# Optimization experiments

Measured on AMD Instinct MI355X. Metric: run time of the kernel, lower is better.

The kernel has to match this reference:

```python
import jax, jax.numpy as jnp
import numpy as np

STRIDES = (8.0, 16.0, 32.0)
NC, DFL = 80, 16
NO = NC + 4 * DFL            # 144
TOPK, ALPHA, BETA, EPS = 10, 0.5, 6.0, 1e-9
MAXB = 32                    # static max gt boxes per image (pad rows are masked out)
W_CLS, W_BOX, W_DFL = 0.5, 7.5, 1.5
B, IMG, NT = 16, 640, 256


def _make_anchors(shapes, strides, offset=0.5):
    pts, strs = [], []
    for (h, w), s in zip(shapes, strides):
        sx = jnp.arange(w, dtype=jnp.float32) + offset
        sy = jnp.arange(h, dtype=jnp.float32) + offset
        gy, gx = jnp.meshgrid(sy, sx, indexing='ij')
        pts.append(jnp.stack([gx, gy], -1).reshape(-1, 2))
        strs.append(jnp.full((h * w, 1), s, dtype=jnp.float32))
    return jnp.concatenate(pts, 0), jnp.concatenate(strs, 0)


def _ciou(box1, box2, eps=1e-7):
    b1x1, b1y1, b1x2, b1y2 = jnp.split(box1, 4, -1)
    b2x1, b2y1, b2x2, b2y2 = jnp.split(box2, 4, -1)
    w1, h1 = b1x2 - b1x1, b1y2 - b1y1 + eps
    w2, h2 = b2x2 - b2x1, b2y2 - b2y1 + eps
    inter = (jnp.maximum(jnp.minimum(b1x2, b2x2) - jnp.maximum(b1x1, b2x1), 0.0) *
             jnp.maximum(jnp.minimum(b1y2, b2y2) - jnp.maximum(b1y1, b2y1), 0.0))
    union = w1 * h1 + w2 * h2 - inter + eps
    iou = inter / union
    cw = jnp.maximum(b1x2, b2x2) - jnp.minimum(b1x1, b2x1)
    ch = jnp.maximum(b1y2, b2y2) - jnp.minimum(b1y1, b2y1)
    c2 = cw ** 2 + ch ** 2 + eps
    rho2 = ((b2x1 + b2x2 - b1x1 - b1x2) ** 2 + (b2y1 + b2y2 - b1y1 - b1y2) ** 2) / 4
    v = (4.0 / np.pi ** 2) * (jnp.arctan(w2 / h2) - jnp.arctan(w1 / h1)) ** 2
    a = jax.lax.stop_gradient(v / (v - iou + (1.0 + eps)))
    return iou - (rho2 / c2 + v * a)     # [..., 1]


def _assign(scores, bboxes, gt_labels, gt_bboxes, mask_gt, anchors):
    # Task-aligned assigner (YOLOv8 TAL). All inputs are gradient-stopped.
    b, a, c = scores.shape
    n = gt_bboxes.shape[1]
    lt, rb = gt_bboxes[..., :2], gt_bboxes[..., 2:]
    deltas = jnp.concatenate([anchors[None, None] - lt[:, :, None],
                              rb[:, :, None] - anchors[None, None]], -1)        # [b,n,a,4]
    mask_in_gts = (deltas.min(-1) > EPS).astype(scores.dtype)                   # [b,n,a]
    overlaps = jnp.maximum(_ciou(gt_bboxes[:, :, None], bboxes[:, None])[..., 0], 0.0)
    labels = gt_labels[..., 0].astype(jnp.int32)                                # [b,n]
    bbox_scores = jax.vmap(lambda s, l: jnp.take(s, l, axis=1).T)(scores, labels)  # [b,n,a]
    align = bbox_scores ** ALPHA * overlaps ** BETA
    mask_true = mask_in_gts * mask_gt                                           # [b,n,a]
    metrics = align * mask_true
    tkv, tki = jax.lax.top_k(metrics, TOPK)                                     # [b,n,k]
    valid = jnp.max(tkv, -1, keepdims=True) > EPS
    tki = jnp.where(valid, tki, 0)
    bi = jnp.arange(b)[:, None, None]
    ni = jnp.arange(n)[None, :, None]
    cnt = jnp.zeros((b, n, a), scores.dtype).at[bi, ni, tki].add(1.0)
    mask_topk = jnp.where(cnt > 1, 0.0, cnt)
    mask_pos = mask_topk * mask_true
    fg = mask_pos.sum(1)                                                        # [b,a]
    multi = (fg > 1)[:, None, :]
    is_max = jnp.transpose(jax.nn.one_hot(jnp.argmax(overlaps, 1), n, dtype=scores.dtype), (0, 2, 1))
    mask_pos = jnp.where(multi, is_max, mask_pos)
    fg = mask_pos.sum(1)
    tgi = jnp.argmax(mask_pos, 1)                                               # [b,a]
    t_labels = jnp.take_along_axis(labels, tgi, axis=1)
    t_bboxes = jnp.take_along_axis(gt_bboxes, jnp.broadcast_to(tgi[..., None], (b, a, 4)), axis=1)
    t_scores = jax.nn.one_hot(jnp.maximum(t_labels, 0), NC, dtype=scores.dtype) * (fg > 0)[..., None]
    align = align * mask_pos
    pos_align = jnp.max(align, -1, keepdims=True)                               # [b,n,1]
    pos_ovl = jnp.max(overlaps * mask_pos, -1, keepdims=True)
    norm = jnp.max(align * pos_ovl / (pos_align + EPS), 1)[..., None]           # [b,a,1]
    return t_bboxes, t_scores * norm, fg > 0


def _forward(p3, p4, p5, targets):
    x = [jnp.transpose(o, (0, 3, 1, 2)) for o in (p3, p4, p5)]                  # NCHW
    b = x[0].shape[0]
    out = jnp.concatenate([o.reshape(b, NO, -1) for o in x], 2)
    pred_dist = jnp.transpose(out[:, :4 * DFL], (0, 2, 1))                      # [b,A,64]
    pred_scores = jnp.transpose(out[:, 4 * DFL:], (0, 2, 1))                    # [b,A,80]
    shapes = [o.shape[2:4] for o in x]
    size = jnp.array(shapes[0], jnp.float32) * STRIDES[0]                       # [H, W] pixels
    anchor_points, stride_tensor = _make_anchors(shapes, STRIDES)
    # per-image padded gt tensor (vectorized replacement of the TF scatter loop)
    img = targets[:, 0].astype(jnp.int32)
    nt = targets.shape[0]
    pos = jnp.arange(nt)
    rank = jnp.sum((img[None, :] == img[:, None]) & (pos[None, :] < pos[:, None]), 1)
    gt = jnp.zeros((b, MAXB, 5), jnp.float32).at[img, rank].set(targets[:, 1:])
    scale = jnp.stack([size[1], size[0], size[1], size[0]])
    xywh = gt[..., 1:5] * scale
    gt_bboxes = jnp.concatenate([xywh[..., :2] - xywh[..., 2:] / 2,
                                 xywh[..., :2] + xywh[..., 2:] / 2], -1)
    gt_labels = gt[..., 0:1]
    mask_gt = (jnp.sum(gt_bboxes, 2, keepdims=True) > 0).astype(jnp.float32)    # [b,n,1]
    a_num = pred_dist.shape[1]
    project = jnp.arange(DFL, dtype=jnp.float32)
    pd = jax.nn.softmax(pred_dist.reshape(b, a_num, 4, DFL), -1)
    pd = jnp.einsum('bafc,c->baf', pd, project)                                 # DFL expectation
    pred_bboxes = jnp.concatenate([anchor_points - pd[..., :2],
                                   anchor_points + pd[..., 2:]], -1)            # [b,A,4]
    scores = jax.lax.stop_gradient(jax.nn.sigmoid(pred_scores))
    bboxes = jax.lax.stop_gradient(pred_bboxes * stride_tensor)
    t_bboxes, t_scores, fg = _assign(scores, bboxes, gt_labels, gt_bboxes, mask_gt,
                                     anchor_points * stride_tensor)
    t_bboxes = t_bboxes / stride_tensor
    tss = jnp.maximum(jnp.sum(t_scores), 1.0)
    z, l = t_scores, pred_scores
    bce = jnp.maximum(l, 0.0) - l * z + jnp.log1p(jnp.exp(-jnp.abs(l)))
    loss_cls = jnp.sum(bce) / tss
    fgf = fg.astype(jnp.float32)
    weight = jnp.sum(t_scores, -1) * fgf                                        # [b,A], 0 off-fg
    iou = _ciou(pred_bboxes, t_bboxes)[..., 0]
    loss_box = jnp.sum((1.0 - iou) * weight) / tss
    lt_rb = jnp.concatenate([anchor_points - t_bboxes[..., :2],
                             t_bboxes[..., 2:] - anchor_points], -1)
    lt_rb = jnp.clip(lt_rb, 0.0, DFL - 1.01)                                    # [b,A,4]
    logp = jax.nn.log_softmax(pred_dist.reshape(b, a_num, 4, DFL), -1)
    tl = lt_rb.astype(jnp.int32)
    wl = (tl + 1).astype(jnp.float32) - lt_rb
    left = -jnp.take_along_axis(logp, tl[..., None], -1)[..., 0]
    right = -jnp.take_along_axis(logp, (tl + 1)[..., None], -1)[..., 0]
    dfl = jnp.mean(left * wl + right * (1.0 - wl), -1)                          # [b,A]
    loss_dfl = jnp.sum(dfl * weight) / tss
    return W_CLS * loss_cls + W_BOX * loss_box + W_DFL * loss_dfl


def setup_inputs() -> dict:
    key = jax.random.key(0)
    k1, k2, k3, k4, k5, k6 = jax.random.split(key, 6)
    p3 = jax.random.normal(k1, (B, IMG // 8, IMG // 8, NO), jnp.float32)
    p4 = jax.random.normal(k2, (B, IMG // 16, IMG // 16, NO), jnp.float32)
    p5 = jax.random.normal(k3, (B, IMG // 32, IMG // 32, NO), jnp.float32)
    img = (jnp.arange(NT) % B).astype(jnp.float32)        # exactly 16 boxes / image <= MAXB
    cls = jax.random.randint(k4, (NT,), 0, NC).astype(jnp.float32)
    xy = jax.random.uniform(k5, (NT, 2), minval=0.25, maxval=0.75)
    wh = jax.random.uniform(k6, (NT, 2), minval=0.05, maxval=0.30)
    targets = jnp.concatenate([img[:, None], cls[:, None], xy, wh], -1)   # [NT,6]
    return {"p3": p3, "p4": p4, "p5": p5, "targets": targets}


def reference(p3, p4, p5, targets):
    return _forward(p3, p4, p5, targets)
```

## Files before the change

### kernel.cpp

```cpp
#include <hip/hip_runtime.h>
#include <math.h>

#define A_TOT 8400
#define NB 16
#define NG 32
#define NCH 144
#define NDFL 16
#define EPSF 1e-9f
#define CEPS 1e-7f
#define INV_PI2_4 0.40528473456935109f
#define NBLK2 2100
#define LSEG 512
#define K56_BLOCKS 32
#define K4CAP 1024

#define LOADU(p)  __hip_atomic_load((p), __ATOMIC_ACQUIRE, __HIP_MEMORY_SCOPE_AGENT)
#define LOADF(p)  __hip_atomic_load((p), __ATOMIC_ACQUIRE, __HIP_MEMORY_SCOPE_AGENT)

#define OFF_GTBOX   0
#define OFF_GTLAB   2048
#define OFF_MASKGT  2560
#define OFF_ATANGT  3072
#define OFF_ACC     3584
#define OFF_CTRL    3592
#define OFF_BCNT    3600
#define OFF_PART2   3856
#define OFF_PART6   5968
#define OFF_POSM    6224
#define OFF_PBOX    10320
#define OFF_MPOS    547920
#define OFF_LIST    682320

__device__ __forceinline__ void locate(int a, int& loc, int& W, float& s, int& lvl, int& hw){
  if (a < 6400)      { lvl = 0; loc = a;        W = 80; s = 8.f;  hw = 6400; }
  else if (a < 8000) { lvl = 1; loc = a - 6400; W = 40; s = 16.f; hw = 1600; }
  else               { lvl = 2; loc = a - 8000; W = 20; s = 32.f; hw = 400;  }
}

__device__ __forceinline__ const float* level_ptr(const float* p3, const float* p4, const float* p5, int lvl){
  return lvl == 0 ? p3 : (lvl == 1 ? p4 : p5);
}

__device__ __forceinline__ float ciou_gp(float gx1,float gy1,float gx2,float gy2,float atg,
                                         float px1,float py1,float px2,float py2,float atp){
  float w1 = gx2-gx1, h1 = gy2-gy1+CEPS;
  float w2 = px2-px1, h2 = py2-py1+CEPS;
  float iw = fmaxf(fminf(gx2,px2)-fmaxf(gx1,px1), 0.f);
  float ih = fmaxf(fminf(gy2,py2)-fmaxf(gy1,py1), 0.f);
  float inter = iw*ih;
  float uni = w1*h1 + w2*h2 - inter + CEPS;
  float iou = inter/uni;
  float cw = fmaxf(gx2,px2)-fminf(gx1,px1);
  float ch = fmaxf(gy2,py2)-fminf(gy1,py1);
  float c2 = cw*cw + ch*ch + CEPS;
  float dx = px1+px2-gx1-gx2, dy = py1+py2-gy1-gy2;
  float rho2 = (dx*dx + dy*dy)*0.25f;
  float dv = atp - atg;
  float v = INV_PI2_4*dv*dv;
  float al = v/(v - iou + (1.f + CEPS));
  return iou - (rho2/c2 + v*al);
}

__global__ __launch_bounds__(256) void k2x(const float* __restrict__ p3, const float* __restrict__ p4,
                          const float* __restrict__ p5, const float* __restrict__ tgt, int nt,
                          float* __restrict__ ws){
  int tid = threadIdx.x;
  int bx = blockIdx.x;
  if (bx == NBLK2){
    __shared__ int simg[256];
    float* gtbox  = ws + OFF_GTBOX;
    int*   gtlab  = (int*)(ws + OFF_GTLAB);
    float* maskgt = ws + OFF_MASKGT;
    float* atangt = ws + OFF_ATANGT;
    for (int i = tid; i < NB*NG*4; i += 256) gtbox[i] = 0.f;
    for (int i = tid; i < NB*NG; i += 256) gtlab[i] = 0;
    if (tid < 8){ (ws + OFF_ACC)[tid] = 0.f; ((unsigned*)(ws + OFF_CTRL))[tid] = 0u; }
    for (int i = tid; i < 256;  i += 256) ((unsigned*)(ws + OFF_BCNT))[i] = 0u;
    for (int i = tid; i < NB*NG*8; i += 256) (ws + OFF_POSM)[i] = 0.f;
    for (int i = tid; i < nt && i < 256; i += 256) simg[i] = (int)tgt[i*6];
    __syncthreads();
    for (int i = tid; i < nt && i < 256; i += 256){
      int b = simg[i];
      int r = 0;
      for (int j = 0; j < i; j++) r += (simg[j] == b);
      if (b >= 0 && b < NB && r < NG){
        float cls = tgt[i*6+1];
        float cx = tgt[i*6+2]*640.f, cy = tgt[i*6+3]*640.f;
        float w  = tgt[i*6+4]*640.f, h  = tgt[i*6+5]*640.f;
        int o = (b*NG + r)*4;
        gtbox[o+0] = cx - 0.5f*w; gtbox[o+1] = cy - 0.5f*h;
        gtbox[o+2] = cx + 0.5f*w; gtbox[o+3] = cy + 0.5f*h;
        gtlab[b*NG + r] = (int)cls;
      }
    }
    __syncthreads();
    for (int i = tid; i < NB*NG; i += 256){
      float x1 = gtbox[i*4], y1 = gtbox[i*4+1], x2 = gtbox[i*4+2], y2 = gtbox[i*4+3];
      maskgt[i] = ((x1+y1+x2+y2) > 0.f) ? 1.f : 0.f;
      atangt[i] = atanf((x2-x1)/(y2-y1+CEPS));
    }
    return;
  }
  __shared__ float redw[4];
  {
    int mp = bx*256 + tid;
    if (mp < NB*A_TOT) ((unsigned*)(ws + OFF_MPOS))[mp] = 0u;
  }
  const float* base; int grow0, hw, W, lvloff;
  if (bx < 1600)      { base = p3; grow0 = bx*64;        hw = 6400; W = 80; lvloff = 0; }
  else if (bx < 2000) { base = p4; grow0 = (bx-1600)*64; hw = 1600; W = 40; lvloff = 6400; }
  else                { base = p5; grow0 = (bx-2000)*64; hw = 400;  W = 20; lvloff = 8000; }

  const float4* src = (const float4*)base + (size_t)grow0*36;
  {
    int r = tid >> 2, f = tid & 3;
    const float4* rp = src + r*36 + f*4;
    float4 v0 = rp[0], v1 = rp[1], v2 = rp[2], v3 = rp[3];
    float m = v0.x;
    m = fmaxf(m, v0.y); m = fmaxf(m, v0.z); m = fmaxf(m, v0.w);
    m = fmaxf(m, v1.x); m = fmaxf(m, v1.y); m = fmaxf(m, v1.z); m = fmaxf(m, v1.w);
    m = fmaxf(m, v2.x); m = fmaxf(m, v2.y); m = fmaxf(m, v2.z); m = fmaxf(m, v2.w);
    m = fmaxf(m, v3.x); m = fmaxf(m, v3.y); m = fmaxf(m, v3.z); m = fmaxf(m, v3.w);
    float e, se, swe;
    e = __expf(v0.x - m); se = e;            swe = 0.f;
    e = __expf(v0.y - m); se += e;           swe += e;
    e = __expf(v0.z - m); se += e;           swe = fmaf(2.f,  e, swe);
    e = __expf(v0.w - m); se += e;           swe = fmaf(3.f,  e, swe);
    e = __expf(v1.x - m); se += e;           swe = fmaf(4.f,  e, swe);
    e = __expf(v1.y - m); se += e;           swe = fmaf(5.f,  e, swe);
    e = __expf(v1.z - m); se += e;           swe = fmaf(6.f,  e, swe);
    e = __expf(v1.w - m); se += e;           swe = fmaf(7.f,  e, swe);
    e = __expf(v2.x - m); se += e;           swe = fmaf(8.f,  e, swe);
    e = __expf(v2.y - m); se += e;           swe = fmaf(9.f,  e, swe);
    e = __expf(v2.z - m); se += e;           swe = fmaf(10.f, e, swe);
    e = __expf(v2.w - m); se += e;           swe = fmaf(11.f, e, swe);
    e = __expf(v3.x - m); se += e;           swe = fmaf(12.f, e, swe);
    e = __expf(v3.y - m); se += e;           swe = fmaf(13.f, e, swe);
    e = __expf(v3.z - m); se += e;           swe = fmaf(14.f, e, swe);
    e = __expf(v3.w - m); se += e;           swe = fmaf(15.f, e, swe);
    float pdf = __fdividef(swe, se);
    float s1 = __shfl_xor(pdf, 1);
    float s2 = __shfl_xor(pdf, 2);
    float s3 = __shfl_xor(pdf, 3);
    if (f == 0){
      int grow = grow0 + r;
      int b = grow / hw, loc = grow - b*hw;
      float ax = (loc % W) + 0.5f, ay = (loc / W) + 0.5f;
      float4 pb;
      pb.x = ax - pdf; pb.y = ay - s1; pb.z = ax + s2; pb.w = ay + s3;
      ((float4*)(ws + OFF_PBOX))[(size_t)b*A_TOT + lvloff + loc] = pb;
    }
  }
  float sp = 0.f;
  #pragma unroll
  for (int i = 0; i < 5; i++){
    int id = i*256 + tid;
    int r = id/20, q = id - r*20;
    float4 v = src[r*36 + 16 + q];
    #pragma unroll
    for (int e2 = 0; e2 < 4; e2++){
      float x = (&v.x)[e2];
      float ex = __expf(-fabsf(x));
      sp += fmaxf(x, 0.f) + __logf(1.f + ex);
    }
  }
  #pragma unroll
  for (int st = 1; st < 64; st <<= 1) sp += __shfl_xor(sp, st);
  int wid = tid >> 6, lane = tid & 63;
  if (lane == 0) redw[wid] = sp;
  __syncthreads();
  if (tid == 0) (ws + OFF_PART2)[bx] = redw[0]+redw[1]+redw[2]+redw[3];
}

__global__ __launch_bounds__(256) void k4x(const float* __restrict__ p3, const float* __restrict__ p4,
                        const float* __restrict__ p5, float* __restrict__ ws){
  __shared__ unsigned long long wtop[4*10];
  int tid = threadIdx.x;
  int lane = tid & 63, wid = tid >> 6;
  int bx = blockIdx.x;
  int b = bx >> 5, n = bx & 31;
  float mk = ws[OFF_MASKGT + b*NG + n];
  if (mk <= 0.f) return;
  int lab = ((const int*)(ws + OFF_GTLAB))[b*NG + n];
  int ch = 64 + lab;
  float atg = ws[OFF_ATANGT + b*NG + n];
  const float* gt = ws + OFF_GTBOX + (b*NG + n)*4;
  float gx1 = gt[0], gy1 = gt[1], gx2 = gt[2], gy2 = gt[3];

  int clo0 = max(0, (int)floorf(gx1*0.125f   - 0.5f));
  int chi0 = min(79,(int)ceilf (gx2*0.125f   - 0.5f));
  int rlo0 = max(0, (int)floorf(gy1*0.125f   - 0.5f));
  int rhi0 = min(79,(int)ceilf (gy2*0.125f   - 0.5f));
  int clo1 = max(0, (int)floorf(gx1*0.0625f  - 0.5f));
  int chi1 = min(39,(int)ceilf (gx2*0.0625f  - 0.5f));
  int rlo1 = max(0, (int)floorf(gy1*0.0625f  - 0.5f));
  int rhi1 = min(39,(int)ceilf (gy2*0.0625f  - 0.5f));
  int clo2 = max(0, (int)floorf(gx1*0.03125f - 0.5f));
  int chi2 = min(19,(int)ceilf (gx2*0.03125f - 0.5f));
  int rlo2 = max(0, (int)floorf(gy1*0.03125f - 0.5f));
  int rhi2 = min(19,(int)ceilf (gy2*0.03125f - 0.5f));
  int nc0 = chi0-clo0+1, nr0 = rhi0-rlo0+1;
  int nc1 = chi1-clo1+1, nr1 = rhi1-rlo1+1;
  int nc2 = chi2-clo2+1, nr2 = rhi2-rlo2+1;
  int cnt0 = (nc0>0 && nr0>0) ? nc0*nr0 : 0;
  int cnt1 = (nc1>0 && nr1>0) ? nc1*nr1 : 0;
  int cnt2 = (nc2>0 && nr2>0) ? nc2*nr2 : 0;
  if (16+cnt0 > K4CAP)           cnt0 = K4CAP-16;
  if (16+cnt0+cnt1 > K4CAP)      cnt1 = K4CAP-16-cnt0;
  if (16+cnt0+cnt1+cnt2 > K4CAP) cnt2 = K4CAP-16-cnt0-cnt1;
  int b1 = 16 + cnt0, b2 = b1 + cnt1;
  int tot = b2 + cnt2;

  unsigned long long key[4];
  #pragma unroll
  for (int j = 0; j < 4; j++){
    key[j] = 0ull;
    int c = j*256 + tid;
    if (c < tot){
      int aidx, loc, W, hw; float s; const float* bp; bool dup = false;
      if (c < 16)     { aidx = c; loc = c; W = 80; s = 8.f;  hw = 6400; bp = p3; }
      else if (c < b1){ int jj = c-16; int rr = jj/nc0; loc = (rlo0+rr)*80 + clo0 + (jj - rr*nc0);
                        aidx = loc;        W = 80; s = 8.f;  hw = 6400; bp = p3; dup = (aidx < 16); }
      else if (c < b2){ int jj = c-b1; int rr = jj/nc1; loc = (rlo1+rr)*40 + clo1 + (jj - rr*nc1);
                        aidx = 6400 + loc; W = 40; s = 16.f; hw = 1600; bp = p4; }
      else            { int jj = c-b2; int rr = jj/nc2; loc = (rlo2+rr)*20 + clo2 + (jj - rr*nc2);
                        aidx = 8000 + loc; W = 20; s = 32.f; hw = 400;  bp = p5; }
      if (!dup){
        float m = 0.f;
        float axi = ((loc % W) + 0.5f)*s, ayi = ((loc / W) + 0.5f)*s;
        float dmin = fminf(fminf(axi-gx1, ayi-gy1), fminf(gx2-axi, gy2-ayi));
        if (dmin > EPSF){
          float4 pg = ((const float4*)(ws + OFF_PBOX))[(size_t)b*A_TOT + aidx];
          float px1 = pg.x*s, py1 = pg.y*s, px2 = pg.z*s, py2 = pg.w*s;
          float atp = atanf((px2-px1)/(py2-py1+CEPS));
          float o = fmaxf(ciou_gp(gx1,gy1,gx2,gy2,atg, px1,py1,px2,py2,atp), 0.f);
          float l = bp[((size_t)b*hw + loc)*NCH + ch];
          float sc = __frcp_rn(1.f + __expf(-l));
          float o2 = o*o;
          m = sqrtf(sc)*o2*o2*o2;
        }
        key[j] = ((unsigned long long)__float_as_uint(m) << 32)
               | (unsigned long long)(0xFFFFFFFFu - (unsigned)aidx);
      }
    }
  }
  for (int k = 0; k < 10; k++){
    unsigned long long bk = key[0];
    #pragma unroll
    for (int j = 1; j < 4; j++) if (key[j] > bk) bk = key[j];
    #pragma unroll
    for (int st = 1; st < 64; st <<= 1){
      unsigned long long ok = __shfl_xor(bk, st);
      if (ok > bk) bk = ok;
    }
    if (lane == 0) wtop[wid*10 + k] = bk;
    #pragma unroll
    for (int j = 0; j < 4; j++) if (key[j] == bk) key[j] = 0ull;
  }
  __syncthreads();
  if (wid == 0){
    unsigned long long mk64 = (lane < 40) ? wtop[lane] : 0ull;
    float top0m = 0.f;
    int mytop = -1;
    for (int k = 0; k < 10; k++){
      unsigned long long bk = mk64;
      #pragma unroll
      for (int st = 1; st < 64; st <<= 1){
        unsigned long long ok = __shfl_xor(bk, st);
        if (ok > bk) bk = ok;
      }
      if (k == 0) top0m = __uint_as_float((unsigned)(bk >> 32));
      if (lane == k) mytop = (int)(0xFFFFFFFFu - (unsigned)(bk & 0xFFFFFFFFull));
      if (mk64 == bk) mk64 = 0ull;
    }
    bool want = (lane < 10) && (top0m > EPSF) && (mytop >= 0) && (mytop < A_TOT);
    if (want){
      int loc, W, lvl, hw; float s;
      locate(mytop, loc, W, s, lvl, hw);
      float axi = ((loc % W) + 0.5f)*s, ayi = ((loc / W) + 0.5f)*s;
      float dmin = fminf(fminf(axi-gx1, ayi-gy1), fminf(gx2-axi, gy2-ayi));
      want = (dmin > EPSF);
    }
    unsigned old = 0u;
    if (want) old = atomicOr((unsigned*)(ws + OFF_MPOS) + (size_t)b*A_TOT + mytop, 1u << n);
    bool w2 = want && (old == 0u);
    unsigned long long m64 = __ballot(w2);
    if (w2){
      int lead = __ffsll((long long)m64) - 1;
      unsigned base = 0;
      if (lane == lead) base = atomicAdd((unsigned*)(ws + OFF_BCNT) + b*16, (unsigned)__popcll(m64));
      base = __shfl(base, lead);
      unsigned slot = base + (unsigned)__popcll(m64 & ((1ull << lane) - 1ull));
      if (slot < LSEG) ((unsigned*)(ws + OFF_LIST))[b*LSEG + slot] = (unsigned)mytop;
    }
  }
}

__global__ __launch_bounds__(256) void k56x(const float* __restrict__ p3, const float* __restrict__ p4,
                        const float* __restrict__ p5, float* __restrict__ ws, float* __restrict__ out){
  __shared__ float redw[16];
  __shared__ float fin[4];
  __shared__ int lastf;
  __shared__ unsigned cnt_s;
  int tid = threadIdx.x;
  int lane = tid & 63, wid = tid >> 6;
  int s_id = blockIdx.x*256 + tid;
  int b = s_id >> 9, i = s_id & (LSEG-1);
  if (tid == 0) cnt_s = (b < NB) ? LOADU((unsigned*)(ws + OFF_BCNT) + b*16) : 0u;
  __syncthreads();
  unsigned cntb = cnt_s;
  bool valid = false; int a = 0;
  if (b < NB && (unsigned)i < cntb && cntb <= LSEG){
    valid = true;
    a = (int)((unsigned*)(ws + OFF_LIST))[b*LSEG + i];
  }
  int ns = 0; float av = 0.f;
  int loc=0, W=80, lvl=0, hw=6400; float sfac=8.f;
  if (valid){
    unsigned bits = ((const unsigned*)(ws + OFF_MPOS))[(size_t)b*A_TOT + a];
    locate(a, loc, W, sfac, lvl, hw);
    float4 pg = ((const float4*)(ws + OFF_PBOX))[(size_t)b*A_TOT + a];
    float px1 = pg.x*sfac, py1 = pg.y*sfac, px2 = pg.z*sfac, py2 = pg.w*sfac;
    float atp = atanf((px2-px1)/(py2-py1+CEPS));
    if (__popc(bits) == 1){ ns = __ffs(bits) - 1; }
    else {
      float bv = -1.f; ns = 0;
      for (int nn = 0; nn < NG; nn++){
        const float* g = ws + OFF_GTBOX + (b*NG + nn)*4;
        float atg = ws[OFF_ATANGT + b*NG + nn];
        float o = fmaxf(ciou_gp(g[0],g[1],g[2],g[3],atg, px1,py1,px2,py2,atp), 0.f);
        if (o > bv){ bv = o; ns = nn; }
      }
    }
    const float* g = ws + OFF_GTBOX + (b*NG + ns)*4;
    float atg = ws[OFF_ATANGT + b*NG + ns];
    float o = fmaxf(ciou_gp(g[0],g[1],g[2],g[3],atg, px1,py1,px2,py2,atp), 0.f);
    int lab = ((const int*)(ws + OFF_GTLAB))[b*NG + ns];
    float l = level_ptr(p3,p4,p5,lvl)[((size_t)b*hw + loc)*NCH + 64 + lab];
    float sc = __frcp_rn(1.f + __expf(-l));
    float o2 = o*o;
    av = sqrtf(sc)*o2*o2*o2;
    unsigned* pm = (unsigned*)(ws + OFF_POSM) + (b*NG + ns)*8;
    atomicMax(pm + 0, __float_as_uint(av));
    atomicMax(pm + 1, __float_as_uint(o));
  }
  if (blockIdx.x == 0){
    float v = 0.f;
    for (int j = tid; j < NBLK2; j += 256) v += (ws + OFF_PART2)[j];
    #pragma unroll
    for (int st = 1; st < 64; st <<= 1) v += __shfl_xor(v, st);
    if (lane == 0) redw[wid] = v;
    __syncthreads();
    if (tid == 0)
      __hip_atomic_store(ws + OFF_ACC + 0, redw[0]+redw[1]+redw[2]+redw[3],
                         __ATOMIC_RELEASE, __HIP_MEMORY_SCOPE_AGENT);
    __syncthreads();
  }
  __syncthreads();
  if (tid == 0){
    __threadfence();
    __hip_atomic_fetch_add((unsigned*)(ws + OFF_CTRL) + 1, 1u,
                           __ATOMIC_ACQ_REL, __HIP_MEMORY_SCOPE_AGENT);
    while (LOADU((unsigned*)(ws + OFF_CTRL) + 1) < K56_BLOCKS){ __builtin_amdgcn_s_sleep(1); }
  }
  __syncthreads();
  __threadfence();
  float bcec = 0.f, boxl = 0.f, dfll = 0.f, tsc = 0.f;
  if (valid){
    unsigned* pm = (unsigned*)(ws + OFF_POSM) + (b*NG + ns)*8;
    float pa = __uint_as_float(LOADU(pm + 0));
    float po = __uint_as_float(LOADU(pm + 1));
    float norm = av * po / (pa + EPSF);
    const float* row = level_ptr(p3,p4,p5,lvl) + ((size_t)b*hw + loc)*NCH;
    int lab = ((const int*)(ws + OFF_GTLAB))[b*NG + ns];
    if (lab < 0) lab = 0;
    tsc = norm;
    bcec = -row[64 + lab]*norm;
    float4 pb = ((const float4*)(ws + OFF_PBOX))[(size_t)b*A_TOT + a];
    const float* g = ws + OFF_GTBOX + (b*NG + ns)*4;
    float inv_s = 1.f/sfac;
    float tx1 = g[0]*inv_s, ty1 = g[1]*inv_s, tx2 = g[2]*inv_s, ty2 = g[3]*inv_s;
    float w1 = pb.z-pb.x, h1 = pb.w-pb.y+CEPS;
    float w2 = tx2-tx1,   h2 = ty2-ty1+CEPS;
    float iw = fmaxf(fminf(pb.z,tx2)-fmaxf(pb.x,tx1), 0.f);
    float ih = fmaxf(fminf(pb.w,ty2)-fmaxf(pb.y,ty1), 0.f);
    float inter = iw*ih;
    float uni = w1*h1 + w2*h2 - inter + CEPS;
    float iou = inter/uni;
    float cw = fmaxf(pb.z,tx2)-fminf(pb.x,tx1);
    float ch = fmaxf(pb.w,ty2)-fminf(pb.y,ty1);
    float c2 = cw*cw + ch*ch + CEPS;
    float dx = tx1+tx2-pb.x-pb.z, dy = ty1+ty2-pb.y-pb.w;
    float rho2 = (dx*dx + dy*dy)*0.25f;
    float dv = atanf(w2/h2) - atanf(w1/h1);
    float v = INV_PI2_4*dv*dv;
    float al = v/(v - iou + (1.f + CEPS));
    float ci = iou - (rho2/c2 + v*al);
    boxl = (1.f - ci)*norm;
    float ax = (loc % W) + 0.5f, ay = (loc / W) + 0.5f;
    float ltrb[4] = {ax - tx1, ay - ty1, tx2 - ax, ty2 - ay};
    float ds = 0.f;
    #pragma unroll
    for (int f = 0; f < 4; f++){
      float val = fminf(fmaxf(ltrb[f], 0.f), (float)NDFL - 1.01f);
      int tl = (int)val;
      float wl = (float)(tl + 1) - val;
      float x[16];
      const float4* r4 = (const float4*)(row + f*16);
      #pragma unroll
      for (int q = 0; q < 4; q++){ float4 vv = r4[q]; x[q*4]=vv.x; x[q*4+1]=vv.y; x[q*4+2]=vv.z; x[q*4+3]=vv.w; }
      float m = x[0];
      #pragma unroll
      for (int j = 1; j < 16; j++) m = fmaxf(m, x[j]);
      float se = 0.f;
      #pragma unroll
      for (int j = 0; j < 16; j++) se += __expf(x[j]-m);
      float lse = m + __logf(se);
      float xl = 0.f, xr = 0.f;
      #pragma unroll
      for (int j = 0; j < 16; j++){
        xl = (j == tl)   ? x[j] : xl;
        xr = (j == tl+1) ? x[j] : xr;
      }
      ds += (lse - xl)*wl + (lse - xr)*(1.f - wl);
    }
    dfll = ds*0.25f*norm;
  }
  float vals[4] = {bcec, boxl, dfll, tsc};
  #pragma unroll
  for (int q = 0; q < 4; q++){
    float v = vals[q];
    #pragma unroll
    for (int st = 1; st < 64; st <<= 1) v += __shfl_xor(v, st);
    if (lane == 0) redw[wid*4 + q] = v;
  }
  if (tid == 0) lastf = 0;
  __syncthreads();
  if (tid < 4){
    float v = redw[tid] + redw[4+tid] + redw[8+tid] + redw[12+tid];
    __hip_atomic_store(ws + OFF_PART6 + blockIdx.x*4 + tid, v,
                       __ATOMIC_RELEASE, __HIP_MEMORY_SCOPE_AGENT);
  }
  __syncthreads();
  if (tid == 0){
    __threadfence();
    unsigned tkt = __hip_atomic_fetch_add((unsigned*)(ws + OFF_CTRL) + 2, 1u,
                                          __ATOMIC_ACQ_REL, __HIP_MEMORY_SCOPE_AGENT);
    if (tkt == K56_BLOCKS - 1) lastf = 1;
  }
  __syncthreads();
  if (lastf){
    if (tid < 4) fin[tid] = 0.f;
    __syncthreads();
    if (tid < 4*K56_BLOCKS){
      float v = LOADF(ws + OFF_PART6 + tid);
      atomicAdd(&fin[tid & 3], v);
    }
    __syncthreads();
    if (tid == 0){
      float sp = LOADF(ws + OFF_ACC + 0);
      float tss = fmaxf(fin[3], 1.f);
      out[0] = (0.5f*(sp + fin[0]) + 7.5f*fin[1] + 1.5f*fin[2]) / tss;
    }
  }
}

extern "C" void kernel_launch(void* const* d_in, const int* in_sizes, int n_in,
                              void* d_out, int out_size, void* d_ws, size_t ws_size,
                              hipStream_t stream) {
  const float* p3 = (const float*)d_in[0];
  const float* p4 = (const float*)d_in[1];
  const float* p5 = (const float*)d_in[2];
  const float* tg = (const float*)d_in[3];
  int nt = in_sizes[3] / 6;
  float* ws = (float*)d_ws;
  float* out = (float*)d_out;

  k2x<<<NBLK2 + 1, 256, 0, stream>>>(p3, p4, p5, tg, nt, ws);
  k4x<<<NB*NG, 256, 0, stream>>>(p3, p4, p5, ws);
  k56x<<<K56_BLOCKS, 256, 0, stream>>>(p3, p4, p5, ws, out);
}
```

Before: 62.84 us.

## Fuse top-k assignment and loss kernels with a grid-wide arrival barrier

Merges the per-GT top-k selection kernel (512 blocks) and the loss kernel (32 blocks) into one launch. The first 32 blocks wait on a set of 16 padded arrival counters until all 512 blocks finish the top-k phase, then run the loss stage. This removes a kernel launch and its inter-kernel gap. The cost is spin-waiting blocks, and correctness depends on all 512 blocks being co-resident or scheduled before the waiters starve them.

New measurement: 85.98 us. +36.8%, slower.

```diff
diff --git a/kernel.cpp b/kernel.cpp
--- a/kernel.cpp
+++ b/kernel.cpp
@@ -11,6 +11,7 @@
 #define INV_PI2_4 0.40528473456935109f
 #define NBLK2 2100
 #define LSEG 512
+#define K46_BLOCKS 512
 #define K56_BLOCKS 32
 #define K4CAP 1024
 
@@ -24,12 +25,13 @@
 #define OFF_ACC     3584
 #define OFF_CTRL    3592
 #define OFF_BCNT    3600
-#define OFF_PART2   3856
-#define OFF_PART6   5968
-#define OFF_POSM    6224
-#define OFF_PBOX    10320
-#define OFF_MPOS    547920
-#define OFF_LIST    682320
+#define OFF_ARR     3856
+#define OFF_PART2   4112
+#define OFF_PART6   6224
+#define OFF_POSM    6352
+#define OFF_PBOX    10448
+#define OFF_MPOS    548048
+#define OFF_LIST    682448
 
 __device__ __forceinline__ void locate(int a, int& loc, int& W, float& s, int& lvl, int& hw){
   if (a < 6400)      { lvl = 0; loc = a;        W = 80; s = 8.f;  hw = 6400; }
@@ -75,7 +77,7 @@
     for (int i = tid; i < NB*NG*4; i += 256) gtbox[i] = 0.f;
     for (int i = tid; i < NB*NG; i += 256) gtlab[i] = 0;
     if (tid < 8){ (ws + OFF_ACC)[tid] = 0.f; ((unsigned*)(ws + OFF_CTRL))[tid] = 0u; }
-    for (int i = tid; i < 256;  i += 256) ((unsigned*)(ws + OFF_BCNT))[i] = 0u;
+    for (int i = tid; i < 512;  i += 256) ((unsigned*)(ws + OFF_BCNT))[i] = 0u;
     for (int i = tid; i < NB*NG*8; i += 256) (ws + OFF_POSM)[i] = 0.f;
     for (int i = tid; i < nt && i < 256; i += 256) simg[i] = (int)tgt[i*6];
     __syncthreads();
@@ -172,139 +174,153 @@
   if (tid == 0) (ws + OFF_PART2)[bx] = redw[0]+redw[1]+redw[2]+redw[3];
 }
 
-__global__ __launch_bounds__(256) void k4x(const float* __restrict__ p3, const float* __restrict__ p4,
-                        const float* __restrict__ p5, float* __restrict__ ws){
+__global__ __launch_bounds__(256) void k46(const float* __restrict__ p3, const float* __restrict__ p4,
+                        const float* __restrict__ p5, float* __restrict__ ws, float* __restrict__ out){
   __shared__ unsigned long long wtop[4*10];
-  int tid = threadIdx.x;
-  int lane = tid & 63, wid = tid >> 6;
-  int bx = blockIdx.x;
-  int b = bx >> 5, n = bx & 31;
-  float mk = ws[OFF_MASKGT + b*NG + n];
-  if (mk <= 0.f) return;
-  int lab = ((const int*)(ws + OFF_GTLAB))[b*NG + n];
-  int ch = 64 + lab;
-  float atg = ws[OFF_ATANGT + b*NG + n];
-  const float* gt = ws + OFF_GTBOX + (b*NG + n)*4;
-  float gx1 = gt[0], gy1 = gt[1], gx2 = gt[2], gy2 = gt[3];
-
-  int clo0 = max(0, (int)floorf(gx1*0.125f   - 0.5f));
-  int chi0 = min(79,(int)ceilf (gx2*0.125f   - 0.5f));
-  int rlo0 = max(0, (int)floorf(gy1*0.125f   - 0.5f));
-  int rhi0 = min(79,(int)ceilf (gy2*0.125f   - 0.5f));
-  int clo1 = max(0, (int)floorf(gx1*0.0625f  - 0.5f));
-  int chi1 = min(39,(int)ceilf (gx2*0.0625f  - 0.5f));
-  int rlo1 = max(0, (int)floorf(gy1*0.0625f  - 0.5f));
-  int rhi1 = min(39,(int)ceilf (gy2*0.0625f  - 0.5f));
-  int clo2 = max(0, (int)floorf(gx1*0.03125f - 0.5f));
-  int chi2 = min(19,(int)ceilf (gx2*0.03125f - 0.5f));
-  int rlo2 = max(0, (int)floorf(gy1*0.03125f - 0.5f));
-  int rhi2 = min(19,(int)ceilf (gy2*0.03125f - 0.5f));
-  int nc0 = chi0-clo0+1, nr0 = rhi0-rlo0+1;
-  int nc1 = chi1-clo1+1, nr1 = rhi1-rlo1+1;
-  int nc2 = chi2-clo2+1, nr2 = rhi2-rlo2+1;
-  int cnt0 = (nc0>0 && nr0>0) ? nc0*nr0 : 0;
-  int cnt1 = (nc1>0 && nr1>0) ? nc1*nr1 : 0;
-  int cnt2 = (nc2>0 && nr2>0) ? nc2*nr2 : 0;
-  if (16+cnt0 > K4CAP)           cnt0 = K4CAP-16;
-  if (16+cnt0+cnt1 > K4CAP)      cnt1 = K4CAP-16-cnt0;
-  if (16+cnt0+cnt1+cnt2 > K4CAP) cnt2 = K4CAP-16-cnt0-cnt1;
-  int b1 = 16 + cnt0, b2 = b1 + cnt1;
-  int tot = b2 + cnt2;
-
-  unsigned long long key[4];
-  #pragma unroll
-  for (int j = 0; j < 4; j++){
-    key[j] = 0ull;
-    int c = j*256 + tid;
-    if (c < tot){
-      int aidx, loc, W, hw; float s; const float* bp; bool dup = false;
-      if (c < 16)     { aidx = c; loc = c; W = 80; s = 8.f;  hw = 6400; bp = p3; }
-      else if (c < b1){ int jj = c-16; int rr = jj/nc0; loc = (rlo0+rr)*80 + clo0 + (jj - rr*nc0);
-                        aidx = loc;        W = 80; s = 8.f;  hw = 6400; bp = p3; dup = (aidx < 16); }
-      else if (c < b2){ int jj = c-b1; int rr = jj/nc1; loc = (rlo1+rr)*40 + clo1 + (jj - rr*nc1);
-                        aidx = 6400 + loc; W = 40; s = 16.f; hw = 1600; bp = p4; }
-      else            { int jj = c-b2; int rr = jj/nc2; loc = (rlo2+rr)*20 + clo2 + (jj - rr*nc2);
-                        aidx = 8000 + loc; W = 20; s = 32.f; hw = 400;  bp = p5; }
-      if (!dup){
-        float m = 0.f;
-        float axi = ((loc % W) + 0.5f)*s, ayi = ((loc / W) + 0.5f)*s;
-        float dmin = fminf(fminf(axi-gx1, ayi-gy1), fminf(gx2-axi, gy2-ayi));
-        if (dmin > EPSF){
-          float4 pg = ((const float4*)(ws + OFF_PBOX))[(size_t)b*A_TOT + aidx];
-          float px1 = pg.x*s, py1 = pg.y*s, px2 = pg.z*s, py2 = pg.w*s;
-          float atp = atanf((px2-px1)/(py2-py1+CEPS));
-          float o = fmaxf(ciou_gp(gx1,gy1,gx2,gy2,atg, px1,py1,px2,py2,atp), 0.f);
-          float l = bp[((size_t)b*hw + loc)*NCH + ch];
-          float sc = __frcp_rn(1.f + __expf(-l));
-          float o2 = o*o;
-          m = sqrtf(sc)*o2*o2*o2;
-        }
-        key[j] = ((unsigned long long)__float_as_uint(m) << 32)
-               | (unsigned long long)(0xFFFFFFFFu - (unsigned)aidx);
-      }
-    }
-  }
-  for (int k = 0; k < 10; k++){
-    unsigned long long bk = key[0];
-    #pragma unroll
-    for (int j = 1; j < 4; j++) if (key[j] > bk) bk = key[j];
-    #pragma unroll
-    for (int st = 1; st < 64; st <<= 1){
-      unsigned long long ok = __shfl_xor(bk, st);
-      if (ok > bk) bk = ok;
-    }
-    if (lane == 0) wtop[wid*10 + k] = bk;
-    #pragma unroll
-    for (int j = 0; j < 4; j++) if (key[j] == bk) key[j] = 0ull;
-  }
-  __syncthreads();
-  if (wid == 0){
-    unsigned long long mk64 = (lane < 40) ? wtop[lane] : 0ull;
-    float top0m = 0.f;
-    int mytop = -1;
-    for (int k = 0; k < 10; k++){
-      unsigned long long bk = mk64;
-      #pragma unroll
-      for (int st = 1; st < 64; st <<= 1){
-        unsigned long long ok = __shfl_xor(bk, st);
-        if (ok > bk) bk = ok;
-      }
-      if (k == 0) top0m = __uint_as_float((unsigned)(bk >> 32));
-      if (lane == k) mytop = (int)(0xFFFFFFFFu - (unsigned)(bk & 0xFFFFFFFFull));
-      if (mk64 == bk) mk64 = 0ull;
-    }
-    bool want = (lane < 10) && (top0m > EPSF) && (mytop >= 0) && (mytop < A_TOT);
-    if (want){
-      int loc, W, lvl, hw; float s;
-      locate(mytop, loc, W, s, lvl, hw);
-      float axi = ((loc % W) + 0.5f)*s, ayi = ((loc / W) + 0.5f)*s;
-      float dmin = fminf(fminf(axi-gx1, ayi-gy1), fminf(gx2-axi, gy2-ayi));
-      want = (dmin > EPSF);
-    }
-    unsigned old = 0u;
-    if (want) old = atomicOr((unsigned*)(ws + OFF_MPOS) + (size_t)b*A_TOT + mytop, 1u << n);
-    bool w2 = want && (old == 0u);
-    unsigned long long m64 = __ballot(w2);
-    if (w2){
-      int lead = __ffsll((long long)m64) - 1;
-      unsigned base = 0;
-      if (lane == lead) base = atomicAdd((unsigned*)(ws + OFF_BCNT) + b*16, (unsigned)__popcll(m64));
-      base = __shfl(base, lead);
-      unsigned slot = base + (unsigned)__popcll(m64 & ((1ull << lane) - 1ull));
-      if (slot < LSEG) ((unsigned*)(ws + OFF_LIST))[b*LSEG + slot] = (unsigned)mytop;
-    }
-  }
-}
-
-__global__ __launch_bounds__(256) void k56x(const float* __restrict__ p3, const float* __restrict__ p4,
-                        const float* __restrict__ p5, float* __restrict__ ws, float* __restrict__ out){
   __shared__ float redw[16];
   __shared__ float fin[4];
   __shared__ int lastf;
   __shared__ unsigned cnt_s;
   int tid = threadIdx.x;
   int lane = tid & 63, wid = tid >> 6;
-  int s_id = blockIdx.x*256 + tid;
+  int bx = blockIdx.x;
+
+  {
+    int b = bx >> 5, n = bx & 31;
+    float mk = ws[OFF_MASKGT + b*NG + n];
+    if (mk > 0.f){
+      int lab = ((const int*)(ws + OFF_GTLAB))[b*NG + n];
+      int ch = 64 + lab;
+      float atg = ws[OFF_ATANGT + b*NG + n];
+      const float* gt = ws + OFF_GTBOX + (b*NG + n)*4;
+      float gx1 = gt[0], gy1 = gt[1], gx2 = gt[2], gy2 = gt[3];
+      int clo0 = max(0, (int)floorf(gx1*0.125f   - 0.5f));
+      int chi0 = min(79,(int)ceilf (gx2*0.125f   - 0.5f));
+      int rlo0 = max(0, (int)floorf(gy1*0.125f   - 0.5f));
+      int rhi0 = min(79,(int)ceilf (gy2*0.125f   - 0.5f));
+      int clo1 = max(0, (int)floorf(gx1*0.0625f  - 0.5f));
+      int chi1 = min(39,(int)ceilf (gx2*0.0625f  - 0.5f));
+      int rlo1 = max(0, (int)floorf(gy1*0.0625f  - 0.5f));
+      int rhi1 = min(39,(int)ceilf (gy2*0.0625f  - 0.5f));
+      int clo2 = max(0, (int)floorf(gx1*0.03125f - 0.5f));
+      int chi2 = min(19,(int)ceilf (gx2*0.03125f - 0.5f));
+      int rlo2 = max(0, (int)floorf(gy1*0.03125f - 0.5f));
+      int rhi2 = min(19,(int)ceilf (gy2*0.03125f - 0.5f));
+      int nc0 = chi0-clo0+1, nr0 = rhi0-rlo0+1;
+      int nc1 = chi1-clo1+1, nr1 = rhi1-rlo1+1;
+      int nc2 = chi2-clo2+1, nr2 = rhi2-rlo2+1;
+      int cnt0 = (nc0>0 && nr0>0) ? nc0*nr0 : 0;
+      int cnt1 = (nc1>0 && nr1>0) ? nc1*nr1 : 0;
+      int cnt2 = (nc2>0 && nr2>0) ? nc2*nr2 : 0;
+      if (16+cnt0 > K4CAP)           cnt0 = K4CAP-16;
+      if (16+cnt0+cnt1 > K4CAP)      cnt1 = K4CAP-16-cnt0;
+      if (16+cnt0+cnt1+cnt2 > K4CAP) cnt2 = K4CAP-16-cnt0-cnt1;
+      int b1 = 16 + cnt0, b2 = b1 + cnt1;
+      int tot = b2 + cnt2;
+      unsigned long long key[4];
+      #pragma unroll
+      for (int j = 0; j < 4; j++){
+        key[j] = 0ull;
+        int c = j*256 + tid;
+        if (c < tot){
+          int aidx, loc, W, hw; float s; const float* bp; bool dup = false;
+          if (c < 16)     { aidx = c; loc = c; W = 80; s = 8.f;  hw = 6400; bp = p3; }
+          else if (c < b1){ int jj = c-16; int rr = jj/nc0; loc = (rlo0+rr)*80 + clo0 + (jj - rr*nc0);
+                            aidx = loc;        W = 80; s = 8.f;  hw = 6400; bp = p3; dup = (aidx < 16); }
+          else if (c < b2){ int jj = c-b1; int rr = jj/nc1; loc = (rlo1+rr)*40 + clo1 + (jj - rr*nc1);
+                            aidx = 6400 + loc; W = 40; s = 16.f; hw = 1600; bp = p4; }
+          else            { int jj = c-b2; int rr = jj/nc2; loc = (rlo2+rr)*20 + clo2 + (jj - rr*nc2);
+                            aidx = 8000 + loc; W = 20; s = 32.f; hw = 400;  bp = p5; }
+          if (!dup){
+            float m = 0.f;
+            float axi = ((loc % W) + 0.5f)*s, ayi = ((loc / W) + 0.5f)*s;
+            float dmin = fminf(fminf(axi-gx1, ayi-gy1), fminf(gx2-axi, gy2-ayi));
+            if (dmin > EPSF){
+              float4 pg = ((const float4*)(ws + OFF_PBOX))[(size_t)b*A_TOT + aidx];
+              float px1 = pg.x*s, py1 = pg.y*s, px2 = pg.z*s, py2 = pg.w*s;
+              float atp = atanf((px2-px1)/(py2-py1+CEPS));
+              float o = fmaxf(ciou_gp(gx1,gy1,gx2,gy2,atg, px1,py1,px2,py2,atp), 0.f);
+              float l = bp[((size_t)b*hw + loc)*NCH + ch];
+              float sc = __frcp_rn(1.f + __expf(-l));
+              float o2 = o*o;
+              m = sqrtf(sc)*o2*o2*o2;
+            }
+            key[j] = ((unsigned long long)__float_as_uint(m) << 32)
+                   | (unsigned long long)(0xFFFFFFFFu - (unsigned)aidx);
+          }
+        }
+      }
+      for (int k = 0; k < 10; k++){
+        unsigned long long bk = key[0];
+        #pragma unroll
+        for (int j = 1; j < 4; j++) if (key[j] > bk) bk = key[j];
+        #pragma unroll
+        for (int st = 1; st < 64; st <<= 1){
+          unsigned long long ok = __shfl_xor(bk, st);
+          if (ok > bk) bk = ok;
+        }
+        if (lane == 0) wtop[wid*10 + k] = bk;
+        #pragma unroll
+        for (int j = 0; j < 4; j++) if (key[j] == bk) key[j] = 0ull;
+      }
+      __syncthreads();
+      if (wid == 0){
+        unsigned long long mk64 = (lane < 40) ? wtop[lane] : 0ull;
+        float top0m = 0.f;
+        int mytop = -1;
+        for (int k = 0; k < 10; k++){
+          unsigned long long bk = mk64;
+          #pragma unroll
+          for (int st = 1; st < 64; st <<= 1){
+            unsigned long long ok = __shfl_xor(bk, st);
+            if (ok > bk) bk = ok;
+          }
+          if (k == 0) top0m = __uint_as_float((unsigned)(bk >> 32));
+          if (lane == k) mytop = (int)(0xFFFFFFFFu - (unsigned)(bk & 0xFFFFFFFFull));
+          if (mk64 == bk) mk64 = 0ull;
+        }
+        bool want = (lane < 10) && (top0m > EPSF) && (mytop >= 0) && (mytop < A_TOT);
+        if (want){
+          int loc, W, lvl, hw; float s;
+          locate(mytop, loc, W, s, lvl, hw);
+          float axi = ((loc % W) + 0.5f)*s, ayi = ((loc / W) + 0.5f)*s;
+          float dmin = fminf(fminf(axi-gx1, ayi-gy1), fminf(gx2-axi, gy2-ayi));
+          want = (dmin > EPSF);
+        }
+        unsigned old = 0u;
+        if (want) old = atomicOr((unsigned*)(ws + OFF_MPOS) + (size_t)b*A_TOT + mytop, 1u << n);
+        bool w2 = want && (old == 0u);
+        unsigned long long m64 = __ballot(w2);
+        if (w2){
+          int lead = __ffsll((long long)m64) - 1;
+          unsigned base = 0;
+          if (lane == lead) base = atomicAdd((unsigned*)(ws + OFF_BCNT) + b*16, (unsigned)__popcll(m64));
+          base = __shfl(base, lead);
+          unsigned slot = base + (unsigned)__popcll(m64 & ((1ull << lane) - 1ull));
+          if (slot < LSEG) ((unsigned*)(ws + OFF_LIST))[b*LSEG + slot] = (unsigned)mytop;
+        }
+      }
+    }
+  }
+  __syncthreads();
+  if (tid == 0){
+    __threadfence();
+    __hip_atomic_fetch_add((unsigned*)(ws + OFF_ARR) + (bx & 15)*16, 1u,
+                           __ATOMIC_ACQ_REL, __HIP_MEMORY_SCOPE_AGENT);
+  }
+  if (bx >= K56_BLOCKS) return;
+  if (tid == 0){
+    for (;;){
+      unsigned sum = 0;
+      #pragma unroll
+      for (int k = 0; k < 16; k++) sum += LOADU((unsigned*)(ws + OFF_ARR) + k*16);
+      if (sum >= K46_BLOCKS) break;
+      __builtin_amdgcn_s_sleep(1);
+    }
+  }
+  __syncthreads();
+  __threadfence();
+  int s_id = bx*256 + tid;
   int b = s_id >> 9, i = s_id & (LSEG-1);
   if (tid == 0) cnt_s = (b < NB) ? LOADU((unsigned*)(ws + OFF_BCNT) + b*16) : 0u;
   __syncthreads();
@@ -344,7 +360,7 @@
     atomicMax(pm + 0, __float_as_uint(av));
     atomicMax(pm + 1, __float_as_uint(o));
   }
-  if (blockIdx.x == 0){
+  if (bx == 0){
     float v = 0.f;
     for (int j = tid; j < NBLK2; j += 256) v += (ws + OFF_PART2)[j];
     #pragma unroll
@@ -438,7 +454,7 @@
   __syncthreads();
   if (tid < 4){
     float v = redw[tid] + redw[4+tid] + redw[8+tid] + redw[12+tid];
-    __hip_atomic_store(ws + OFF_PART6 + blockIdx.x*4 + tid, v,
+    __hip_atomic_store(ws + OFF_PART6 + bx*4 + tid, v,
                        __ATOMIC_RELEASE, __HIP_MEMORY_SCOPE_AGENT);
   }
   __syncthreads();
@@ -477,6 +493,5 @@
   float* out = (float*)d_out;
 
   k2x<<<NBLK2 + 1, 256, 0, stream>>>(p3, p4, p5, tg, nt, ws);
-  k4x<<<NB*NG, 256, 0, stream>>>(p3, p4, p5, ws);
-  k56x<<<K56_BLOCKS, 256, 0, stream>>>(p3, p4, p5, ws, out);
-}
+  k46<<<K46_BLOCKS, 256, 0, stream>>>(p3, p4, p5, ws, out);
+}
```
